# Kernel optimization log

Hardware: AMD Instinct MI355X
Metric: run time of the kernel (lower is better)

## Reference

```python
import jax, jax.numpy as jnp
import numpy as np

N = 100000
E = 3200000
D_IN = 128
D_OUT = 128
EPS = 1e-5


def setup_inputs() -> dict:
    key = jax.random.key(0)
    ks = jax.random.split(key, 8)
    x = jax.random.normal(ks[0], (N, D_IN), dtype=jnp.float32)
    edge_index = jax.random.randint(ks[1], (2, E), 0, N, dtype=jnp.int32)
    # SAGEConv params: lin_l (neighbor path, has bias), lin_r (root path, no bias)
    s = 1.0 / np.sqrt(D_IN)
    W_l = jax.random.uniform(ks[2], (D_IN, D_OUT), jnp.float32, -s, s)
    b_l = jax.random.uniform(ks[3], (D_OUT,), jnp.float32, -s, s)
    W_r = jax.random.uniform(ks[4], (D_IN, D_OUT), jnp.float32, -s, s)
    # LayerNorm params
    gamma = jnp.ones((D_OUT,), jnp.float32)
    beta = jnp.zeros((D_OUT,), jnp.float32)
    return {"x": x, "edge_index": edge_index, "W_l": W_l, "b_l": b_l,
            "W_r": W_r, "gamma": gamma, "beta": beta}


def reference(x, edge_index, W_l, b_l, W_r, gamma, beta):
    src = edge_index[0]  # message sources
    dst = edge_index[1]  # aggregation targets
    n = x.shape[0]
    # mean aggregation over in-neighbors (SAGEConv default aggr='mean')
    summed = jax.ops.segment_sum(x[src], dst, num_segments=n)  # [N, D_IN]
    deg = jax.ops.segment_sum(jnp.ones((src.shape[0],), x.dtype), dst,
                              num_segments=n)
    mean_neigh = summed / jnp.maximum(deg, 1.0)[:, None]
    # SAGEConv: lin_l(mean_neigh) + lin_r(x)
    h = mean_neigh @ W_l + b_l + x @ W_r  # [N, D_OUT]
    # LayerNorm over last dim
    mu = jnp.mean(h, axis=-1, keepdims=True)
    var = jnp.mean(jnp.square(h - mu), axis=-1, keepdims=True)
    h = (h - mu) * jax.lax.rsqrt(var + EPS) * gamma + beta
    # exact (erf-based) GELU, matching torch nn.GELU default
    return jax.nn.gelu(h, approximate=False)
```

## Files before the change

### kernel.cpp

```cpp
#include <hip/hip_runtime.h>
#include <cstdint>
#include <cstddef>

#define NN 100000
#define NE 3200000
#define D 128

#define NBUK  1563
#define NBUKP 2048
#define BCAP  2560
#define HCAP  1600
#define EPB   12800
#define PBLK  250
#define CBLK  1563
#define GSTR  16

#define EW_OFFMASK 0x00FFFF80u
#define EW_INVALID 0xFFFFFFFFu

typedef __attribute__((ext_vector_type(8))) short bf16x8;
typedef __attribute__((ext_vector_type(4))) float f32x4;
typedef __attribute__((ext_vector_type(2))) float f32x2;

__device__ __forceinline__ unsigned short f2bf(float f) {
    unsigned int u = __float_as_uint(f);
    u += 0x7FFFu + ((u >> 16) & 1u);
    return (unsigned short)(u >> 16);
}

__device__ __forceinline__ bf16x8 fp8x8_to_bf16x8(unsigned int lo, unsigned int hi) {
    const f32x2 p0 = __builtin_amdgcn_cvt_pk_f32_fp8(lo, false);
    const f32x2 p1 = __builtin_amdgcn_cvt_pk_f32_fp8(lo, true);
    const f32x2 p2 = __builtin_amdgcn_cvt_pk_f32_fp8(hi, false);
    const f32x2 p3 = __builtin_amdgcn_cvt_pk_f32_fp8(hi, true);
    union { unsigned int w[4]; bf16x8 v; } r;
    r.w[0] = (unsigned)f2bf(p0[0]) | ((unsigned)f2bf(p0[1]) << 16);
    r.w[1] = (unsigned)f2bf(p1[0]) | ((unsigned)f2bf(p1[1]) << 16);
    r.w[2] = (unsigned)f2bf(p2[0]) | ((unsigned)f2bf(p2[1]) << 16);
    r.w[3] = (unsigned)f2bf(p3[0]) | ((unsigned)f2bf(p3[1]) << 16);
    return r.v;
}

__global__ __launch_bounds__(1024)
void k_all(const float* __restrict__ x,
           const int* __restrict__ ei,
           const float* __restrict__ Wl, const float* __restrict__ Wr,
           unsigned char* __restrict__ xq,
           unsigned short* __restrict__ wf,
           unsigned int* __restrict__ gcur,
           unsigned int* __restrict__ ebuf)
{
    const int blk = blockIdx.x;
    const int t   = threadIdx.x;

    if (blk >= PBLK) {
        if (blk < PBLK + CBLK) {
            const size_t i8 = ((size_t)(blk - PBLK) * 1024 + t) * 8;
            if (i8 < (size_t)NN * D) {
                const float4 v0 = *reinterpret_cast<const float4*>(x + i8);
                const float4 v1 = *reinterpret_cast<const float4*>(x + i8 + 4);
                int p0 = __builtin_amdgcn_cvt_pk_fp8_f32(v0.x, v0.y, 0, false);
                p0     = __builtin_amdgcn_cvt_pk_fp8_f32(v0.z, v0.w, p0, true);
                int p1 = __builtin_amdgcn_cvt_pk_fp8_f32(v1.x, v1.y, 0, false);
                p1     = __builtin_amdgcn_cvt_pk_fp8_f32(v1.z, v1.w, p1, true);
                uint2 q; q.x = (unsigned)p0; q.y = (unsigned)p1;
                *reinterpret_cast<uint2*>(xq + i8) = q;
            }
        } else {
            const int tid  = (blk - PBLK - CBLK) * 1024 + t;
            const int j    = tid & 7;
            const int lane = (tid >> 3) & 63;
            const int tt   = (tid >> 9) & 7;
            const int kt   = tid >> 12;
            const int k    = kt * 32 + (lane >> 4) * 8 + j;
            const int cc   = tt * 16 + (lane & 15);
            const float v  = (k < D) ? Wl[k * D + cc] : Wr[(k - D) * D + cc];
            wf[tid] = f2bf(v);
        }
        return;
    }

    __shared__ unsigned int staging[EPB];
    __shared__ unsigned int hist[NBUKP];
    __shared__ unsigned int wsum[16];

    const int w    = t >> 6;
    const int lane = t & 63;
    const int e0 = blk * EPB;

    hist[t] = 0u; hist[t + 1024] = 0u;
    __syncthreads();

    int dreg[13];
    #pragma unroll
    for (int j = 0; j < 13; ++j) {
        const int e = j * 1024 + t;
        if (e < EPB) {
            dreg[j] = ei[NE + e0 + e];
            atomicAdd(&hist[dreg[j] >> 6], 1u);
        }
    }
    __syncthreads();

    const unsigned int c = hist[t * 2] + hist[t * 2 + 1];
    unsigned int p = c;
    #pragma unroll
    for (int d = 1; d < 64; d <<= 1) {
        const unsigned int v = __shfl_up(p, d, 64);
        if (lane >= d) p += v;
    }
    if (lane == 63) wsum[w] = p;
    __syncthreads();
    if (t < 16) {
        const unsigned int s = wsum[t];
        unsigned int q = s;
        #pragma unroll
        for (int d = 1; d < 16; d <<= 1) {
            const unsigned int v = __shfl_up(q, d, 16);
            if (t >= d) q += v;
        }
        wsum[t] = q - s;
    }
    __syncthreads();
    unsigned int running = wsum[w] + (p - c);
    #pragma unroll
    for (int k = 0; k < 2; ++k) {
        running += hist[t * 2 + k];
        hist[t * 2 + k] = running;
    }
    __syncthreads();

    #pragma unroll
    for (int j = 0; j < 13; ++j) {
        const int e = j * 1024 + t;
        if (e < EPB) {
            const int s = ei[e0 + e];
            const int d = dreg[j];
            const unsigned int pos = atomicSub(&hist[d >> 6], 1u) - 1u;
            staging[pos] = ((unsigned)(d & 63) << 25) | ((unsigned)s << 7);
        }
    }
    __syncthreads();

    int i = (t * 25) >> 1;
    const int wEnd = ((t + 1) * 25) >> 1;
    int lo = 0, hi = NBUKP - 1;
    while (lo < hi) {
        const int mid = (lo + hi + 1) >> 1;
        if ((int)hist[mid] <= i) lo = mid; else hi = mid - 1;
    }
    int bp = lo;
    while (i < wEnd) {
        while (bp + 1 < NBUKP && (int)hist[bp + 1] <= i) ++bp;
        const int bEnd = (bp + 1 < NBUKP) ? (int)hist[bp + 1] : EPB;
        const int runEnd = (wEnd < bEnd) ? wEnd : bEnd;
        const int len = runEnd - i;
        const unsigned int g = atomicAdd(&gcur[bp * GSTR], (unsigned)len);
        if (g + (unsigned)len <= (unsigned)BCAP) {
            unsigned int dj = (unsigned)bp * BCAP + g;
            int k = 0;
            if ((dj & 1u) && k < len) { ebuf[dj] = staging[i + k]; ++k; ++dj; }
            for (; k + 1 < len; k += 2, dj += 2) {
                uint2 pr; pr.x = staging[i + k]; pr.y = staging[i + k + 1];
                *reinterpret_cast<uint2*>(&ebuf[dj]) = pr;
            }
            if (k < len) ebuf[dj] = staging[i + k];
        }
        i = runEnd;
    }
}

__global__ __launch_bounds__(256, 8)
void k_gather(const unsigned char* __restrict__ xq,
              const unsigned int* __restrict__ gcur,
              const unsigned int* __restrict__ ebuf,
              unsigned int* __restrict__ meanbuf)
{
    __shared__ unsigned int ew[HCAP];
    __shared__ unsigned int hcnt[64];
    __shared__ unsigned int hstart[65];

    const int t    = threadIdx.x;
    const int w    = t >> 6;
    const int lane = t & 63;
    const int b    = blockIdx.x >> 1;
    const int h    = blockIdx.x & 1;

    const unsigned int cntu = gcur[b * GSTR];
    const int count = (int)(cntu < (unsigned)BCAP ? cntu : (unsigned)BCAP);
    const size_t bb = (size_t)b * BCAP;

    unsigned int wreg[10];
    #pragma unroll
    for (int k = 0; k < 10; ++k) {
        const int i = t + k * 256;
        wreg[k] = (i < count) ? ebuf[bb + i] : EW_INVALID;
    }
    if (t < 64) hcnt[t] = 0u;
    __syncthreads();

    #pragma unroll
    for (int k = 0; k < 10; ++k)
        if (wreg[k] != EW_INVALID) atomicAdd(&hcnt[wreg[k] >> 25], 1u);
    __syncthreads();

    if (t < 64) {
        unsigned int p = hcnt[t];
        #pragma unroll
        for (int d = 1; d < 64; d <<= 1) {
            const unsigned int v = __shfl_up(p, d, 64);
            if (lane >= d) p += v;
        }
        hstart[t + 1] = p;
        if (t == 0) hstart[0] = 0u;
    }
    __syncthreads();
    const unsigned int base = hstart[h * 32];
    if (t < 64) hcnt[t] = hstart[t] - base;
    __syncthreads();

    #pragma unroll
    for (int k = 0; k < 10; ++k) {
        const unsigned int wv = wreg[k];
        if (wv != EW_INVALID) {
            const unsigned int n = wv >> 25;
            if ((int)(n >> 5) == h) {
                const unsigned int pos = atomicAdd(&hcnt[n], 1u);
                if (pos < (unsigned)HCAP) ew[pos] = wv;
            }
        }
    }
    __syncthreads();

    const int half = lane >> 5;
    const int hl   = lane & 31;
    const unsigned char* xqb = xq + (hl << 2);

    for (int i = 0; i < 8; ++i) {
        const int n = h * 32 + w * 8 + i;
        int s = (int)(hstart[n] - base);
        int e = (int)(hstart[n + 1] - base);
        if (e > HCAP) e = HCAP;
        if (s > e) s = e;
        const int dg = e - s;
        f32x2 acc01 = {0.f, 0.f};
        f32x2 acc23 = {0.f, 0.f};
        int c = s;
        for (; c + 8 <= e; c += 8) {
            unsigned int u[4];
            #pragma unroll
            for (int j = 0; j < 4; ++j) {
                const unsigned int wj = ew[c + 2 * j + half];
                u[j] = *reinterpret_cast<const unsigned int*>(xqb + (wj & EW_OFFMASK));
            }
            #pragma unroll
            for (int j = 0; j < 4; ++j) {
                acc01 += __builtin_amdgcn_cvt_pk_f32_fp8(u[j], false);
                acc23 += __builtin_amdgcn_cvt_pk_f32_fp8(u[j], true);
            }
        }
        for (; c + 2 <= e; c += 2) {
            const unsigned int w0 = ew[c + half];
            const unsigned int u0 = *reinterpret_cast<const unsigned int*>(xqb + (w0 & EW_OFFMASK));
            acc01 += __builtin_amdgcn_cvt_pk_f32_fp8(u0, false);
            acc23 += __builtin_amdgcn_cvt_pk_f32_fp8(u0, true);
        }
        if (c < e && half == 0) {
            const unsigned int w0 = ew[c];
            const unsigned int u0 = *reinterpret_cast<const unsigned int*>(xqb + (w0 & EW_OFFMASK));
            acc01 += __builtin_amdgcn_cvt_pk_f32_fp8(u0, false);
            acc23 += __builtin_amdgcn_cvt_pk_f32_fp8(u0, true);
        }
        float a0 = acc01[0], a1 = acc01[1], a2 = acc23[0], a3 = acc23[1];
        a0 += __shfl_xor(a0, 32, 64);
        a1 += __shfl_xor(a1, 32, 64);
        a2 += __shfl_xor(a2, 32, 64);
        a3 += __shfl_xor(a3, 32, 64);
        const float inv = 1.0f / (float)(dg > 1 ? dg : 1);
        if (half == 0) {
            int pk = __builtin_amdgcn_cvt_pk_fp8_f32(a0 * inv, a1 * inv, 0, false);
            pk     = __builtin_amdgcn_cvt_pk_fp8_f32(a2 * inv, a3 * inv, pk, true);
            meanbuf[((size_t)b * 64 + n) * 32 + hl] = (unsigned)pk;
        }
    }
}

__global__ __launch_bounds__(256)
void k_gemm(const float* __restrict__ x,
            const unsigned int* __restrict__ meanbuf,
            const unsigned short* __restrict__ wf,
            const float* __restrict__ bl,
            const float* __restrict__ gamma,
            const float* __restrict__ beta,
            float* __restrict__ out)
{
    __shared__ unsigned char smean[64][136];

    const int t    = threadIdx.x;
    const int w    = t >> 6;
    const int lane = t & 63;
    const int b    = blockIdx.x;
    const int nodeBase = b * 64;

    const unsigned int* gm = meanbuf + (size_t)b * 2048;
    #pragma unroll
    for (int k = 0; k < 8; ++k) {
        const int idx = k * 256 + t;
        const int row = idx >> 5;
        const int c4  = (idx & 31) << 2;
        *reinterpret_cast<unsigned int*>(&smean[row][c4]) = gm[idx];
    }
    __syncthreads();

    const int row  = lane & 15;
    const int kgrp = lane >> 4;
    const int node_r = nodeBase + w * 16 + row;
    const float* xp = x + ((size_t)(node_r < NN ? node_r : NN - 1) << 7);

    f32x4 accr[8];
    const f32x4 zero = {0.f, 0.f, 0.f, 0.f};
    #pragma unroll
    for (int q = 0; q < 8; ++q) accr[q] = zero;

    #pragma unroll
    for (int kt = 0; kt < 8; ++kt) {
        bf16x8 a;
        if (kt < 4) {
            const uint2 m8 = *reinterpret_cast<const uint2*>(
                &smean[w * 16 + row][kt * 32 + kgrp * 8]);
            a = fp8x8_to_bf16x8(m8.x, m8.y);
        } else {
            const float4 va = *reinterpret_cast<const float4*>(
                xp + (kt - 4) * 32 + kgrp * 8);
            const float4 vb = *reinterpret_cast<const float4*>(
                xp + (kt - 4) * 32 + kgrp * 8 + 4);
            union { unsigned int wd[4]; bf16x8 v; } r;
            r.wd[0] = (unsigned)f2bf(va.x) | ((unsigned)f2bf(va.y) << 16);
            r.wd[1] = (unsigned)f2bf(va.z) | ((unsigned)f2bf(va.w) << 16);
            r.wd[2] = (unsigned)f2bf(vb.x) | ((unsigned)f2bf(vb.y) << 16);
            r.wd[3] = (unsigned)f2bf(vb.z) | ((unsigned)f2bf(vb.w) << 16);
            a = r.v;
        }
        #pragma unroll
        for (int q = 0; q < 8; ++q) {
            const bf16x8 bfrag = *reinterpret_cast<const bf16x8*>(
                wf + (((kt * 8 + q) * 64 + lane) << 3));
            accr[q] = __builtin_amdgcn_mfma_f32_16x16x32_bf16(a, bfrag, accr[q], 0, 0, 0);
        }
    }

    const int col = lane & 15;
    float gv[8], bev[8], blv[8];
    #pragma unroll
    for (int q = 0; q < 8; ++q) {
        gv[q]  = gamma[q * 16 + col];
        bev[q] = beta[q * 16 + col];
        blv[q] = bl[q * 16 + col];
    }
    const float k2 = 0.70710678118654752f;
    #pragma unroll
    for (int r = 0; r < 4; ++r) {
        float p = 0.f, p2 = 0.f;
        #pragma unroll
        for (int q = 0; q < 8; ++q) {
            const float h = accr[q][r] + blv[q];
            p += h; p2 += h * h;
        }
        #pragma unroll
        for (int m = 1; m <= 8; m <<= 1) {
            p  += __shfl_xor(p,  m, 64);
            p2 += __shfl_xor(p2, m, 64);
        }
        const float mu   = p * (1.0f / 128.0f);
        const float var  = p2 * (1.0f / 128.0f) - mu * mu;
        const float rstd = rsqrtf(var + 1e-5f);
        const int node = nodeBase + w * 16 + kgrp * 4 + r;
        if (node < NN) {
            #pragma unroll
            for (int q = 0; q < 8; ++q) {
                const float h = accr[q][r] + blv[q];
                const float y = (h - mu) * rstd * gv[q] + bev[q];
                out[(size_t)node * D + q * 16 + col] = 0.5f * y * (1.0f + erff(y * k2));
            }
        }
    }
}

extern "C" void kernel_launch(void* const* d_in, const int* in_sizes, int n_in,
                              void* d_out, int out_size, void* d_ws, size_t ws_size,
                              hipStream_t stream)
{
    const float* x     = (const float*)d_in[0];
    const int*   ei    = (const int*)d_in[1];
    const float* Wl    = (const float*)d_in[2];
    const float* bl    = (const float*)d_in[3];
    const float* Wr    = (const float*)d_in[4];
    const float* gamma = (const float*)d_in[5];
    const float* beta  = (const float*)d_in[6];
    float* out = (float*)d_out;

    char* wsp = (char*)d_ws;
    unsigned int*   gcur    = (unsigned int*)(wsp + 0);
    unsigned int*   ebuf    = (unsigned int*)(wsp + 131072);
    unsigned char*  xq      = (unsigned char*)(wsp + 16136192);
    unsigned short* wf      = (unsigned short*)(wsp + 28936192);
    unsigned int*   meanbuf = (unsigned int*)(wsp + 29001728);

    hipMemsetAsync(gcur, 0, (size_t)NBUKP * GSTR * sizeof(unsigned int), stream);

    k_all<<<PBLK + CBLK + 32, 1024, 0, stream>>>(x, ei, Wl, Wr, xq, wf,
                                                 gcur, ebuf);

    k_gather<<<NBUK * 2, 256, 0, stream>>>(xq, gcur, ebuf, meanbuf);

    k_gemm<<<NBUK, 256, 0, stream>>>(x, meanbuf, wf, bl, gamma, beta, out);
}
```

Baseline: 150.1 us.

## Widen destination buckets to 128 nodes and split gather into quarter-bucket blocks

Destination nodes are now binned into 782 buckets of 128 nodes instead of 1563 buckets of 64, with a larger per-bucket edge capacity. The binning kernel's histogram and scan shrink to one entry per thread. The gather kernel launches four blocks per bucket, each handling 32 nodes, so each block reads twice as many edge words and filters them. Fewer buckets mean fewer global atomic runs and fewer partial writes during binning. In exchange the gather side does more redundant edge reads and needs more registers, with occupancy lowered from 8 to 6 blocks.

```diff
diff --git a/kernel.cpp b/kernel.cpp
--- a/kernel.cpp
+++ b/kernel.cpp
@@ -6,9 +6,9 @@
 #define NE 3200000
 #define D 128
 
-#define NBUK  1563
-#define NBUKP 2048
-#define BCAP  2560
+#define NBUK  782
+#define NBUKP 1024
+#define BCAP  4608
 #define HCAP  1600
 #define EPB   12800
 #define PBLK  250
@@ -88,7 +88,7 @@
     const int lane = t & 63;
     const int e0 = blk * EPB;
 
-    hist[t] = 0u; hist[t + 1024] = 0u;
+    hist[t] = 0u;
     __syncthreads();
 
     int dreg[13];
@@ -97,12 +97,12 @@
         const int e = j * 1024 + t;
         if (e < EPB) {
             dreg[j] = ei[NE + e0 + e];
-            atomicAdd(&hist[dreg[j] >> 6], 1u);
-        }
-    }
-    __syncthreads();
-
-    const unsigned int c = hist[t * 2] + hist[t * 2 + 1];
+            atomicAdd(&hist[dreg[j] >> 7], 1u);
+        }
+    }
+    __syncthreads();
+
+    const unsigned int c = hist[t];
     unsigned int p = c;
     #pragma unroll
     for (int d = 1; d < 64; d <<= 1) {
@@ -122,12 +122,7 @@
         wsum[t] = q - s;
     }
     __syncthreads();
-    unsigned int running = wsum[w] + (p - c);
-    #pragma unroll
-    for (int k = 0; k < 2; ++k) {
-        running += hist[t * 2 + k];
-        hist[t * 2 + k] = running;
-    }
+    hist[t] = wsum[w] + p;
     __syncthreads();
 
     #pragma unroll
@@ -136,8 +131,8 @@
         if (e < EPB) {
             const int s = ei[e0 + e];
             const int d = dreg[j];
-            const unsigned int pos = atomicSub(&hist[d >> 6], 1u) - 1u;
-            staging[pos] = ((unsigned)(d & 63) << 25) | ((unsigned)s << 7);
+            const unsigned int pos = atomicSub(&hist[d >> 7], 1u) - 1u;
+            staging[pos] = ((unsigned)(d & 127) << 25) | ((unsigned)s << 7);
         }
     }
     __syncthreads();
@@ -170,62 +165,66 @@
     }
 }
 
-__global__ __launch_bounds__(256, 8)
+__global__ __launch_bounds__(256, 6)
 void k_gather(const unsigned char* __restrict__ xq,
               const unsigned int* __restrict__ gcur,
               const unsigned int* __restrict__ ebuf,
               unsigned int* __restrict__ meanbuf)
 {
     __shared__ unsigned int ew[HCAP];
-    __shared__ unsigned int hcnt[64];
-    __shared__ unsigned int hstart[65];
+    __shared__ unsigned int hcnt[32];
+    __shared__ unsigned int hstart[33];
 
     const int t    = threadIdx.x;
     const int w    = t >> 6;
     const int lane = t & 63;
-    const int b    = blockIdx.x >> 1;
-    const int h    = blockIdx.x & 1;
+    const int b    = blockIdx.x >> 2;
+    const int q    = blockIdx.x & 3;
 
     const unsigned int cntu = gcur[b * GSTR];
     const int count = (int)(cntu < (unsigned)BCAP ? cntu : (unsigned)BCAP);
     const size_t bb = (size_t)b * BCAP;
 
-    unsigned int wreg[10];
-    #pragma unroll
-    for (int k = 0; k < 10; ++k) {
+    unsigned int wreg[18];
+    #pragma unroll
+    for (int k = 0; k < 18; ++k) {
         const int i = t + k * 256;
         wreg[k] = (i < count) ? ebuf[bb + i] : EW_INVALID;
     }
-    if (t < 64) hcnt[t] = 0u;
-    __syncthreads();
-
-    #pragma unroll
-    for (int k = 0; k < 10; ++k)
-        if (wreg[k] != EW_INVALID) atomicAdd(&hcnt[wreg[k] >> 25], 1u);
-    __syncthreads();
-
-    if (t < 64) {
-        unsigned int p = hcnt[t];
-        #pragma unroll
-        for (int d = 1; d < 64; d <<= 1) {
-            const unsigned int v = __shfl_up(p, d, 64);
-            if (lane >= d) p += v;
-        }
-        hstart[t + 1] = p;
-        if (t == 0) hstart[0] = 0u;
-    }
-    __syncthreads();
-    const unsigned int base = hstart[h * 32];
-    if (t < 64) hcnt[t] = hstart[t] - base;
-    __syncthreads();
-
-    #pragma unroll
-    for (int k = 0; k < 10; ++k) {
+    if (t < 32) hcnt[t] = 0u;
+    __syncthreads();
+
+    #pragma unroll
+    for (int k = 0; k < 18; ++k) {
         const unsigned int wv = wreg[k];
         if (wv != EW_INVALID) {
             const unsigned int n = wv >> 25;
-            if ((int)(n >> 5) == h) {
-                const unsigned int pos = atomicAdd(&hcnt[n], 1u);
+            if ((int)(n >> 5) == q) atomicAdd(&hcnt[n & 31], 1u);
+        }
+    }
+    __syncthreads();
+
+    if (t < 32) {
+        unsigned int p = hcnt[t];
+        #pragma unroll
+        for (int d = 1; d < 32; d <<= 1) {
+            const unsigned int v = __shfl_up(p, d, 64);
+            if (t >= d) p += v;
+        }
+        hstart[t + 1] = p;
+        if (t == 0) hstart[0] = 0u;
+    }
+    __syncthreads();
+    if (t < 32) hcnt[t] = hstart[t];
+    __syncthreads();
+
+    #pragma unroll
+    for (int k = 0; k < 18; ++k) {
+        const unsigned int wv = wreg[k];
+        if (wv != EW_INVALID) {
+            const unsigned int n = wv >> 25;
+            if ((int)(n >> 5) == q) {
+                const unsigned int pos = atomicAdd(&hcnt[n & 31], 1u);
                 if (pos < (unsigned)HCAP) ew[pos] = wv;
             }
         }
@@ -237,9 +236,9 @@
     const unsigned char* xqb = xq + (hl << 2);
 
     for (int i = 0; i < 8; ++i) {
-        const int n = h * 32 + w * 8 + i;
-        int s = (int)(hstart[n] - base);
-        int e = (int)(hstart[n + 1] - base);
+        const int l = w * 8 + i;
+        int s = (int)hstart[l];
+        int e = (int)hstart[l + 1];
         if (e > HCAP) e = HCAP;
         if (s > e) s = e;
         const int dg = e - s;
@@ -280,7 +279,8 @@
         if (half == 0) {
             int pk = __builtin_amdgcn_cvt_pk_fp8_f32(a0 * inv, a1 * inv, 0, false);
             pk     = __builtin_amdgcn_cvt_pk_fp8_f32(a2 * inv, a3 * inv, pk, true);
-            meanbuf[((size_t)b * 64 + n) * 32 + hl] = (unsigned)pk;
+            const int node = b * 128 + q * 32 + l;
+            meanbuf[(size_t)node * 32 + hl] = (unsigned)pk;
         }
     }
 }
@@ -402,16 +402,16 @@
     char* wsp = (char*)d_ws;
     unsigned int*   gcur    = (unsigned int*)(wsp + 0);
     unsigned int*   ebuf    = (unsigned int*)(wsp + 131072);
-    unsigned char*  xq      = (unsigned char*)(wsp + 16136192);
-    unsigned short* wf      = (unsigned short*)(wsp + 28936192);
-    unsigned int*   meanbuf = (unsigned int*)(wsp + 29001728);
+    unsigned char*  xq      = (unsigned char*)(wsp + 14544896);
+    unsigned short* wf      = (unsigned short*)(wsp + 27344896);
+    unsigned int*   meanbuf = (unsigned int*)(wsp + 27410432);
 
     hipMemsetAsync(gcur, 0, (size_t)NBUKP * GSTR * sizeof(unsigned int), stream);
 
     k_all<<<PBLK + CBLK + 32, 1024, 0, stream>>>(x, ei, Wl, Wr, xq, wf,
                                                  gcur, ebuf);
 
-    k_gather<<<NBUK * 2, 256, 0, stream>>>(xq, gcur, ebuf, meanbuf);
-
-    k_gemm<<<NBUK, 256, 0, stream>>>(x, meanbuf, wf, bl, gamma, beta, out);
-}
+    k_gather<<<NBUK * 4, 256, 0, stream>>>(xq, gcur, ebuf, meanbuf);
+
+    k_gemm<<<1564, 256, 0, stream>>>(x, meanbuf, wf, bl, gamma, beta, out);
+}
```

After: 146.2 us, median of 2. 2.6% less time.
